# Kernel optimization log

Measured on AMD Instinct MI355X. Metric: run time of the kernel, lower is better.

## Reference

```python
import jax, jax.numpy as jnp
import numpy as np

B, S, D = 4, 1024, 1024
H, DK, DV = 16, 64, 64


def setup_inputs() -> dict:
    key = jax.random.key(0)
    ks = jax.random.split(key, 8)
    sc = 0.02
    return {
        "queries": jax.random.normal(ks[0], (B, S, D), jnp.float32),
        "keys": jax.random.normal(ks[1], (B, S, D), jnp.float32),
        "values": jax.random.normal(ks[2], (B, S, D), jnp.float32),
        "attn_bias": jax.random.normal(ks[3], (B, 1, S, S), jnp.float32),
        "Wq": jax.random.normal(ks[4], (H * DK, D), jnp.float32) * sc,
        "Wk": jax.random.normal(ks[5], (H * DK, D), jnp.float32) * sc,
        "Wv": jax.random.normal(ks[6], (H * DV, D), jnp.float32) * sc,
        "Wp": jax.random.normal(ks[7], (D, H * DV), jnp.float32) * sc,
    }


def reference(queries, keys, values, attn_bias, Wq, Wk, Wv, Wp):
    # Linear (no bias): x @ W.T, then split heads -> [B, H, S, d]
    q = (queries @ Wq.T).reshape(B, S, H, DK).transpose(0, 2, 1, 3)
    k = (keys @ Wk.T).reshape(B, S, H, DK).transpose(0, 2, 1, 3)
    v = (values @ Wv.T).reshape(B, S, H, DV).transpose(0, 2, 1, 3)
    # NOTE: original scales by d_model**-0.5, not d_key**-0.5
    scores = jnp.einsum("bhqd,bhkd->bhqk", q, k) * (D ** -0.5)
    scores = scores + attn_bias  # bias broadcasts over heads
    weights = jax.nn.softmax(scores, axis=-1)
    out = jnp.einsum("bhqk,bhkd->bhqd", weights, v)  # [B,H,S,DV]
    out = out.transpose(0, 2, 1, 3).reshape(B, S, H * DV)
    return out @ Wp.T
```

## Files before the change

### kernel.cpp

```cpp
#include <hip/hip_runtime.h>
#include <hip/hip_bf16.h>

typedef unsigned short u16;
typedef unsigned int u32;
typedef __attribute__((ext_vector_type(8))) short bf16x8;
typedef __attribute__((ext_vector_type(8))) u16 u16x8;
typedef __attribute__((ext_vector_type(4))) u16 u16x4;
typedef __attribute__((ext_vector_type(4))) u32 u32x4;
typedef __attribute__((ext_vector_type(4))) float f32x4;
typedef __attribute__((ext_vector_type(4))) _Float16 f16x4;
typedef __attribute__((ext_vector_type(16))) float f32x16;

typedef const __attribute__((address_space(1))) void* gas1_t;
typedef __attribute__((address_space(3))) void* las3_t;

#define MFMA16(a,b,c) __builtin_amdgcn_mfma_f32_16x16x32_bf16((a),(b),(c),0,0,0)
#define MFMA32(a,b,c) __builtin_amdgcn_mfma_f32_32x32x16_bf16((a),(b),(c),0,0,0)

static constexpr int BB = 4, SS = 1024, DD = 1024, HH = 16;

static __device__ __forceinline__ u16 f2b(float x) {
  union { __hip_bfloat16 h; u16 u; } cv;
  cv.h = __float2bfloat16(x);
  return cv.u;
}
static __device__ __forceinline__ u32 pk2(float a, float b) {
  return (u32)f2b(a) | ((u32)f2b(b) << 16);
}

__global__ __launch_bounds__(256) void cvt_all(
    const float* __restrict__ q, const float* __restrict__ k, const float* __restrict__ v,
    const float* __restrict__ wq_, const float* __restrict__ wk_, const float* __restrict__ wv_,
    const float* __restrict__ wp_,
    u16* __restrict__ qb, u16* __restrict__ kb, u16* __restrict__ vb,
    u16* __restrict__ wqb, u16* __restrict__ wkb, u16* __restrict__ wvb, u16* __restrict__ wpb) {
  int bid = blockIdx.x;
  const float* s; u16* d; int off;
  if      (bid < 4096)  { s = q;   d = qb;  off = bid; }
  else if (bid < 8192)  { s = k;   d = kb;  off = bid - 4096; }
  else if (bid < 12288) { s = v;   d = vb;  off = bid - 8192; }
  else if (bid < 13312) { s = wq_; d = wqb; off = bid - 12288; }
  else if (bid < 14336) { s = wk_; d = wkb; off = bid - 13312; }
  else if (bid < 15360) { s = wv_; d = wvb; off = bid - 14336; }
  else                  { s = wp_; d = wpb; off = bid - 15360; }
  int i = (off * 256 + threadIdx.x) * 4;
  float4 val = *(const float4*)(s + i);
  u16x4 r = { f2b(val.x), f2b(val.y), f2b(val.z), f2b(val.w) };
  *(u16x4*)(d + i) = r;
}

__global__ __launch_bounds__(256) void cvt_bias(const float* __restrict__ src,
                                                _Float16* __restrict__ dst) {
  int i = (blockIdx.x * 256 + threadIdx.x) * 4;
  float4 v = *(const float4*)(src + i);
  f16x4 r = { (_Float16)v.x, (_Float16)v.y, (_Float16)v.z, (_Float16)v.w };
  *(f16x4*)(dst + i) = r;
}

template<typename OT, bool VTRANS>
__global__ __launch_bounds__(256) void gemm_bt(
    const u16* __restrict__ Abase, const u16* __restrict__ Wbase, OT* __restrict__ Cbase,
    u16* __restrict__ Tout, int N, int K, size_t sA, size_t sW, size_t sC) {
  const u16* A = Abase + (size_t)blockIdx.z * sA;
  const u16* W = Wbase + (size_t)blockIdx.z * sW;
  OT* C = Cbase + (size_t)blockIdx.z * sC;

  __shared__ __align__(16) u16 As[128 * 64];
  __shared__ __align__(16) u16 Bs[128 * 64];

  const int tid = threadIdx.x;
  const int lane = tid & 63;
  const int wid = tid >> 6;
  const int g = lane >> 4;
  const int li = lane & 15;

  const int hw = blockIdx.x + (blockIdx.y << 3);
  const int L = ((hw & 7) << 5) + (hw >> 3);
  const int brow = (L >> 3) * 128;
  const int bcol = (L & 7) * 128;

  const int wr = (wid >> 1) * 64;
  const int wc = (wid & 1) * 64;

  const int srow = wid * 8 + (lane >> 3);
  const int schunk = (lane & 7) ^ (lane >> 3);
  const u16* ga0 = A + (size_t)(brow + srow) * K + schunk * 8;
  const u16* gw0 = W + (size_t)(bcol + srow) * K + schunk * 8;

  f32x4 acc[4][4] = {};

  for (int k0 = 0; k0 < K; k0 += 64) {
#pragma unroll
    for (int i = 0; i < 4; ++i) {
      __builtin_amdgcn_global_load_lds((gas1_t)(const void*)(ga0 + (size_t)(i * 32) * K + k0),
                                       (las3_t)(void*)(As + (i * 32 + wid * 8) * 64), 16, 0, 0);
      __builtin_amdgcn_global_load_lds((gas1_t)(const void*)(gw0 + (size_t)(i * 32) * K + k0),
                                       (las3_t)(void*)(Bs + (i * 32 + wid * 8) * 64), 16, 0, 0);
    }
    __syncthreads();

#pragma unroll
    for (int kk = 0; kk < 2; ++kk) {
      bf16x8 a[4], b[4];
#pragma unroll
      for (int m = 0; m < 4; ++m) {
        int row = wr + m * 16 + li;
        a[m] = *(const bf16x8*)&As[row * 64 + (((kk * 4 + g) ^ (li & 7)) << 3)];
      }
#pragma unroll
      for (int n = 0; n < 4; ++n) {
        int row = wc + n * 16 + li;
        b[n] = *(const bf16x8*)&Bs[row * 64 + (((kk * 4 + g) ^ (li & 7)) << 3)];
      }
#pragma unroll
      for (int m = 0; m < 4; ++m)
#pragma unroll
        for (int n = 0; n < 4; ++n)
          acc[m][n] = MFMA16(a[m], b[n], acc[m][n]);
    }
    __syncthreads();
  }

  if (VTRANS && blockIdx.z == 2) {
#pragma unroll
    for (int m = 0; m < 4; ++m) {
#pragma unroll
      for (int n = 0; n < 4; ++n) {
        int c = bcol + wc + n * 16 + li;
        int h_ = c >> 6, dv = c & 63;
        int r0 = brow + wr + m * 16 + g * 4;
        int b_ = r0 >> 10, s0 = r0 & 1023;
        u16x4 val = { f2b(acc[m][n][0]), f2b(acc[m][n][1]),
                      f2b(acc[m][n][2]), f2b(acc[m][n][3]) };
        *(u16x4*)&Tout[(size_t)((b_ * HH + h_) * 64 + dv) * SS + s0] = val;
      }
    }
  } else {
#pragma unroll
    for (int m = 0; m < 4; ++m)
#pragma unroll
      for (int n = 0; n < 4; ++n)
#pragma unroll
        for (int j = 0; j < 4; ++j) {
          int r = brow + wr + m * 16 + g * 4 + j;
          int c = bcol + wc + n * 16 + li;
          if constexpr (sizeof(OT) == 2) C[(size_t)r * N + c] = (OT)f2b(acc[m][n][j]);
          else                           C[(size_t)r * N + c] = acc[m][n][j];
        }
  }
}

__global__ __launch_bounds__(256) void attn_kernel(
    const u16* __restrict__ Q, const u16* __restrict__ K, const u16* __restrict__ Vt,
    const _Float16* __restrict__ bias16, u16* __restrict__ O) {
  __shared__ __align__(16) u16 kbuf[2][64 * 64];
  __shared__ __align__(16) u16 vbuf[2][64 * 64];
  __shared__ __align__(16) u16 bbuf[2][8192];

  const int tid = threadIdx.x;
  const int lane = tid & 63;
  const int wq = tid >> 6;
  const int hi = lane >> 5;
  const int ln = lane & 31;
  const u32 swz = (u32)(ln & 7) << 4;

  const int flat = blockIdx.x + (blockIdx.y << 3) + (blockIdx.z << 7);
  const int L = ((flat & 7) << 6) | (flat >> 3);
  const int qt = L & 7, h = (L >> 3) & 15, b = L >> 7;
  const int q0 = qt * 128;
  const int qrow = q0 + wq * 32 + ln;

  bf16x8 qf[4];
  {
    const u16* qp = Q + (size_t)(b * SS + qrow) * DD + h * 64 + hi * 8;
#pragma unroll
    for (int d = 0; d < 4; ++d) qf[d] = *(const bf16x8*)(qp + d * 16);
  }

  const int sr = tid >> 2;
  const int scb = (tid & 3) * 32;
  const u16* kg = K + (size_t)(b * SS + sr) * DD + h * 64 + scb / 2;
  const u16* vg = Vt + (size_t)((b * HH + h) * 64 + sr) * SS + scb / 2;
  const u32 wa0 = (u32)sr * 128 + (((u32)scb) ^ ((u32)(sr & 7) << 4));
  const u32 wa1 = (u32)sr * 128 + (((u32)scb + 16) ^ ((u32)(sr & 7) << 4));

  const int r_l = lane >> 3;
  const int gl = (lane & 7) ^ r_l;
  const _Float16* bsrc = bias16 + (size_t)(b * SS + q0 + wq * 8 + r_l) * SS + gl * 8;

  const int qq = wq * 32 + ln;
  int baddr[2][4];
#pragma unroll
  for (int kb = 0; kb < 2; ++kb)
#pragma unroll
    for (int rq = 0; rq < 4; ++rq)
      baddr[kb][rq] = qq * 128 + (((kb * 4 + rq) ^ (ln & 7)) << 4) + hi * 8;

  {
    char* bd = (char*)bbuf[0] + wq * 1024;
#pragma unroll
    for (int i = 0; i < 4; ++i)
      __builtin_amdgcn_global_load_lds((gas1_t)(const void*)(bsrc + (size_t)i * 32 * SS),
                                       (las3_t)(void*)(bd + i * 4096), 16, 0, 0);
  }
  u16x8 kr0, kr1, vr0, vr1;
  kr0 = *(const u16x8*)(kg + 0);
  kr1 = *(const u16x8*)(kg + 8);
  vr0 = *(const u16x8*)(vg + 0);
  vr1 = *(const u16x8*)(vg + 8);
  *(u16x8*)((char*)kbuf[0] + wa0) = kr0;
  *(u16x8*)((char*)kbuf[0] + wa1) = kr1;
  *(u16x8*)((char*)vbuf[0] + wa0) = vr0;
  *(u16x8*)((char*)vbuf[0] + wa1) = vr1;
  __syncthreads();

  f32x16 o0 = {}, o1 = {};
  float m = -1e30f, lsum = 0.f;
  int cur = 0;

  for (int kt = 0; kt < 16; ++kt) {
    if (kt < 15) {
      char* bd = (char*)bbuf[cur ^ 1] + wq * 1024;
      const _Float16* bs = bsrc + (kt + 1) * 64;
#pragma unroll
      for (int i = 0; i < 4; ++i)
        __builtin_amdgcn_global_load_lds((gas1_t)(const void*)(bs + (size_t)i * 32 * SS),
                                         (las3_t)(void*)(bd + i * 4096), 16, 0, 0);
      const size_t k1 = (size_t)(kt + 1) * 64;
      kr0 = *(const u16x8*)(kg + k1 * DD + 0);
      kr1 = *(const u16x8*)(kg + k1 * DD + 8);
      vr0 = *(const u16x8*)(vg + k1 + 0);
      vr1 = *(const u16x8*)(vg + k1 + 8);
    }

    const char* kb_base = (const char*)kbuf[cur];
    f32x16 s[2];
#pragma unroll
    for (int kb = 0; kb < 2; ++kb) {
      f32x16 acc = {};
#pragma unroll
      for (int d = 0; d < 4; ++d) {
        bf16x8 kf = *(const bf16x8*)(kb_base + (kb * 32 + ln) * 128 + (((u32)(d * 32 + hi * 16)) ^ swz));
        acc = MFMA32(kf, qf[d], acc);
      }
      s[kb] = acc;
    }

    const char* bbr = (const char*)bbuf[cur];
#pragma unroll
    for (int kb = 0; kb < 2; ++kb)
#pragma unroll
      for (int rq = 0; rq < 4; ++rq) {
        f16x4 bv = *(const f16x4*)(bbr + baddr[kb][rq]);
#pragma unroll
        for (int c = 0; c < 4; ++c)
          s[kb][rq * 4 + c] = fmaf(s[kb][rq * 4 + c], 0.03125f, (float)bv[c]);
      }

    float mt = -1e30f;
#pragma unroll
    for (int r = 0; r < 16; ++r) { mt = fmaxf(mt, s[0][r]); mt = fmaxf(mt, s[1][r]); }
    mt = fmaxf(mt, __shfl_xor(mt, 32));

    bool resc = false;
    float fsc = 1.f;
    if (kt == 0) {
      m = mt;
    } else if (__any(mt > m + 8.f)) {
      float mn = fmaxf(m, mt);
      fsc = __expf(m - mn);
      m = mn;
      resc = true;
    }

    float rs = 0.f;
    u32 wv[2][8];
#pragma unroll
    for (int kb = 0; kb < 2; ++kb)
#pragma unroll
      for (int t = 0; t < 8; ++t) {
        float p0 = __expf(s[kb][2 * t] - m);
        float p1 = __expf(s[kb][2 * t + 1] - m);
        rs += p0 + p1;
        wv[kb][t] = pk2(p0, p1);
      }
    rs += __shfl_xor(rs, 32);
    lsum = lsum * fsc + rs;

    if (resc) {
#pragma unroll
      for (int j = 0; j < 16; ++j) {
        float fv = __shfl(fsc, (j & 3) + 8 * (j >> 2) + 4 * hi);
        o0[j] *= fv; o1[j] *= fv;
      }
    }

    const char* vb_base = (const char*)vbuf[cur];
#pragma unroll
    for (int ks = 0; ks < 4; ++ks) {
      const int kb = ks >> 1, i0 = (ks & 1) * 4;
      u32 sA = hi ? wv[kb][i0 + 0] : wv[kb][i0 + 2];
      u32 sB = hi ? wv[kb][i0 + 1] : wv[kb][i0 + 3];
      u32 rA = (u32)__shfl_xor((int)sA, 32);
      u32 rB = (u32)__shfl_xor((int)sB, 32);
      u32 e0 = hi ? rA : wv[kb][i0 + 0];
      u32 e1 = hi ? rB : wv[kb][i0 + 1];
      u32 e2 = hi ? wv[kb][i0 + 2] : rA;
      u32 e3 = hi ? wv[kb][i0 + 3] : rB;
      union { u32x4 u; bf16x8 v; } pc;
      pc.u = (u32x4){e0, e1, e2, e3};
      bf16x8 pa = pc.v;
#pragma unroll
      for (int nv = 0; nv < 2; ++nv) {
        bf16x8 vf = *(const bf16x8*)(vb_base + (nv * 32 + ln) * 128 + (((u32)(ks * 32 + hi * 16)) ^ swz));
        if (nv == 0) o0 = MFMA32(pa, vf, o0);
        else         o1 = MFMA32(pa, vf, o1);
      }
    }

    if (kt < 15) {
      char* kd = (char*)kbuf[cur ^ 1];
      char* vd = (char*)vbuf[cur ^ 1];
      *(u16x8*)(kd + wa0) = kr0;
      *(u16x8*)(kd + wa1) = kr1;
      *(u16x8*)(vd + wa0) = vr0;
      *(u16x8*)(vd + wa1) = vr1;
      __syncthreads();
      cur ^= 1;
    }
  }

  float inv = 1.0f / lsum;
#pragma unroll
  for (int j = 0; j < 16; ++j) {
    float iv = __shfl(inv, (j & 3) + 8 * (j >> 2) + 4 * hi);
    int q = q0 + wq * 32 + (j & 3) + 8 * (j >> 2) + 4 * hi;
    u16* op = O + (size_t)(b * SS + q) * DD + h * 64 + ln;
    op[0]  = f2b(o0[j] * iv);
    op[32] = f2b(o1[j] * iv);
  }
}

extern "C" void kernel_launch(void* const* d_in, const int* in_sizes, int n_in,
                              void* d_out, int out_size, void* d_ws, size_t ws_size,
                              hipStream_t stream) {
  const float* queries = (const float*)d_in[0];
  const float* keys    = (const float*)d_in[1];
  const float* values  = (const float*)d_in[2];
  const float* bias    = (const float*)d_in[3];
  const float* Wq      = (const float*)d_in[4];
  const float* Wk      = (const float*)d_in[5];
  const float* Wv      = (const float*)d_in[6];
  const float* Wp      = (const float*)d_in[7];
  float* out = (float*)d_out;

  char* ws = (char*)d_ws;
  const size_t MB = 1024 * 1024;
  u16* qb  = (u16*)(ws + 0 * MB);
  u16* kb  = (u16*)(ws + 8 * MB);
  u16* vb  = (u16*)(ws + 16 * MB);
  u16* wqb = (u16*)(ws + 24 * MB);
  u16* wkb = (u16*)(ws + 26 * MB);
  u16* wvb = (u16*)(ws + 28 * MB);
  u16* wpb = (u16*)(ws + 30 * MB);
  u16* Qb  = (u16*)(ws + 32 * MB);
  u16* Kb  = (u16*)(ws + 40 * MB);
  u16* Vtb = (u16*)(ws + 56 * MB);
  _Float16* bias16 = (_Float16*)(ws + 8 * MB);
  u16* Ob  = (u16*)(ws + 0 * MB);

  const int nAct = BB * SS * DD;
  const int nW = DD * DD;

  cvt_all<<<dim3(16384), dim3(256), 0, stream>>>(
      queries, keys, values, Wq, Wk, Wv, Wp,
      qb, kb, vb, wqb, wkb, wvb, wpb);

  gemm_bt<u16, true><<<dim3(8, 32, 3), dim3(256), 0, stream>>>(
      qb, wqb, Qb, Vtb, DD, DD, (size_t)nAct, (size_t)nW, (size_t)nAct);

  cvt_bias<<<dim3(4096), dim3(256), 0, stream>>>(bias, bias16);

  attn_kernel<<<dim3(8, 16, 4), dim3(256), 0, stream>>>(Qb, Kb, Vtb, bias16, Ob);

  gemm_bt<float, false><<<dim3(8, 32, 1), dim3(256), 0, stream>>>(
      Ob, wpb, out, nullptr, DD, DD, 0, 0, 0);
}
```

Before: 118.1 us.

## Load K/V tiles via direct global-to-LDS and pre-permute bias layout

K and V tiles are now fetched with global_load_lds straight into shared memory using a swizzled lane mapping, instead of staging through registers and writing to LDS at the end of each iteration. The bias conversion kernel now writes fp16 bias in a permuted, swizzled order so the attention kernel can read 8 halves per LDS load instead of 4. This removes register pressure and VALU/LDS-store work from the inner loop and halves bias LDS reads. It depends on the new bias layout matching the MFMA accumulator ordering exactly.

```diff
diff --git a/kernel.cpp b/kernel.cpp
--- a/kernel.cpp
+++ b/kernel.cpp
@@ -9,6 +9,7 @@
 typedef __attribute__((ext_vector_type(4))) u32 u32x4;
 typedef __attribute__((ext_vector_type(4))) float f32x4;
 typedef __attribute__((ext_vector_type(4))) _Float16 f16x4;
+typedef __attribute__((ext_vector_type(8))) _Float16 f16x8;
 typedef __attribute__((ext_vector_type(16))) float f32x16;
 
 typedef const __attribute__((address_space(1))) void* gas1_t;
@@ -52,9 +53,16 @@
 __global__ __launch_bounds__(256) void cvt_bias(const float* __restrict__ src,
                                                 _Float16* __restrict__ dst) {
   int i = (blockIdx.x * 256 + threadIdx.x) * 4;
+  int row = i >> 10;
+  int k = i & 1023;
+  int kt = k >> 6, j = k & 63;
+  int hi = (j >> 2) & 1, kb = j >> 5, rq = (j >> 3) & 3;
+  int idx = hi * 32 + kb * 16 + rq * 4;
+  int byte_in_slice = ((((idx >> 3) ^ (row & 7)) << 4) | ((idx & 7) << 1));
   float4 v = *(const float4*)(src + i);
   f16x4 r = { (_Float16)v.x, (_Float16)v.y, (_Float16)v.z, (_Float16)v.w };
-  *(f16x4*)(dst + i) = r;
+  char* p = (char*)dst + ((size_t)row * 1024 + kt * 64) * 2 + byte_in_slice;
+  *(f16x4*)p = r;
 }
 
 template<typename OT, bool VTRANS>
@@ -177,41 +185,35 @@
     for (int d = 0; d < 4; ++d) qf[d] = *(const bf16x8*)(qp + d * 16);
   }
 
-  const int sr = tid >> 2;
-  const int scb = (tid & 3) * 32;
-  const u16* kg = K + (size_t)(b * SS + sr) * DD + h * 64 + scb / 2;
-  const u16* vg = Vt + (size_t)((b * HH + h) * 64 + sr) * SS + scb / 2;
-  const u32 wa0 = (u32)sr * 128 + (((u32)scb) ^ ((u32)(sr & 7) << 4));
-  const u32 wa1 = (u32)sr * 128 + (((u32)scb + 16) ^ ((u32)(sr & 7) << 4));
-
-  const int r_l = lane >> 3;
-  const int gl = (lane & 7) ^ r_l;
-  const _Float16* bsrc = bias16 + (size_t)(b * SS + q0 + wq * 8 + r_l) * SS + gl * 8;
+  const int srow = (lane >> 3);
+  const int spc = ((lane & 7) ^ srow) * 8;
+  const u16* kgl = K + (size_t)(b * SS + wq * 16 + srow) * DD + h * 64 + spc;
+  const u16* vgl = Vt + (size_t)((b * HH + h) * 64 + wq * 16 + srow) * SS + spc;
+
+  const _Float16* bgl = bias16 + (size_t)(b * SS + q0 + wq * 32 + srow) * SS + (lane & 7) * 8;
 
   const int qq = wq * 32 + ln;
-  int baddr[2][4];
-#pragma unroll
-  for (int kb = 0; kb < 2; ++kb)
-#pragma unroll
-    for (int rq = 0; rq < 4; ++rq)
-      baddr[kb][rq] = qq * 128 + (((kb * 4 + rq) ^ (ln & 7)) << 4) + hi * 8;
+  int baddr[4];
+#pragma unroll
+  for (int g = 0; g < 4; ++g)
+    baddr[g] = qq * 128 + (((hi * 4 + g) ^ (ln & 7)) << 4);
 
   {
-    char* bd = (char*)bbuf[0] + wq * 1024;
+    char* bd = (char*)bbuf[0] + wq * 4096;
 #pragma unroll
     for (int i = 0; i < 4; ++i)
-      __builtin_amdgcn_global_load_lds((gas1_t)(const void*)(bsrc + (size_t)i * 32 * SS),
-                                       (las3_t)(void*)(bd + i * 4096), 16, 0, 0);
-  }
-  u16x8 kr0, kr1, vr0, vr1;
-  kr0 = *(const u16x8*)(kg + 0);
-  kr1 = *(const u16x8*)(kg + 8);
-  vr0 = *(const u16x8*)(vg + 0);
-  vr1 = *(const u16x8*)(vg + 8);
-  *(u16x8*)((char*)kbuf[0] + wa0) = kr0;
-  *(u16x8*)((char*)kbuf[0] + wa1) = kr1;
-  *(u16x8*)((char*)vbuf[0] + wa0) = vr0;
-  *(u16x8*)((char*)vbuf[0] + wa1) = vr1;
+      __builtin_amdgcn_global_load_lds((gas1_t)(const void*)(bgl + (size_t)(i * 8) * SS),
+                                       (las3_t)(void*)(bd + i * 1024), 16, 0, 0);
+    char* kd = (char*)kbuf[0] + wq * 2048;
+    char* vd = (char*)vbuf[0] + wq * 2048;
+#pragma unroll
+    for (int j = 0; j < 2; ++j) {
+      __builtin_amdgcn_global_load_lds((gas1_t)(const void*)(kgl + (size_t)(j * 8) * DD),
+                                       (las3_t)(void*)(kd + j * 1024), 16, 0, 0);
+      __builtin_amdgcn_global_load_lds((gas1_t)(const void*)(vgl + (size_t)(j * 8) * SS),
+                                       (las3_t)(void*)(vd + j * 1024), 16, 0, 0);
+    }
+  }
   __syncthreads();
 
   f32x16 o0 = {}, o1 = {};
@@ -220,17 +222,22 @@
 
   for (int kt = 0; kt < 16; ++kt) {
     if (kt < 15) {
-      char* bd = (char*)bbuf[cur ^ 1] + wq * 1024;
-      const _Float16* bs = bsrc + (kt + 1) * 64;
+      char* bd = (char*)bbuf[cur ^ 1] + wq * 4096;
+      const _Float16* bs = bgl + (kt + 1) * 64;
 #pragma unroll
       for (int i = 0; i < 4; ++i)
-        __builtin_amdgcn_global_load_lds((gas1_t)(const void*)(bs + (size_t)i * 32 * SS),
-                                         (las3_t)(void*)(bd + i * 4096), 16, 0, 0);
+        __builtin_amdgcn_global_load_lds((gas1_t)(const void*)(bs + (size_t)(i * 8) * SS),
+                                         (las3_t)(void*)(bd + i * 1024), 16, 0, 0);
+      char* kd = (char*)kbuf[cur ^ 1] + wq * 2048;
+      char* vd = (char*)vbuf[cur ^ 1] + wq * 2048;
       const size_t k1 = (size_t)(kt + 1) * 64;
-      kr0 = *(const u16x8*)(kg + k1 * DD + 0);
-      kr1 = *(const u16x8*)(kg + k1 * DD + 8);
-      vr0 = *(const u16x8*)(vg + k1 + 0);
-      vr1 = *(const u16x8*)(vg + k1 + 8);
+#pragma unroll
+      for (int j = 0; j < 2; ++j) {
+        __builtin_amdgcn_global_load_lds((gas1_t)(const void*)(kgl + (k1 + j * 8) * DD),
+                                         (las3_t)(void*)(kd + j * 1024), 16, 0, 0);
+        __builtin_amdgcn_global_load_lds((gas1_t)(const void*)(vgl + (size_t)(j * 8) * SS + k1),
+                                         (las3_t)(void*)(vd + j * 1024), 16, 0, 0);
+      }
     }
 
     const char* kb_base = (const char*)kbuf[cur];
@@ -246,16 +253,18 @@
       s[kb] = acc;
     }
 
-    const char* bbr = (const char*)bbuf[cur];
-#pragma unroll
-    for (int kb = 0; kb < 2; ++kb)
-#pragma unroll
-      for (int rq = 0; rq < 4; ++rq) {
-        f16x4 bv = *(const f16x4*)(bbr + baddr[kb][rq]);
-#pragma unroll
-        for (int c = 0; c < 4; ++c)
-          s[kb][rq * 4 + c] = fmaf(s[kb][rq * 4 + c], 0.03125f, (float)bv[c]);
-      }
+    {
+      const char* bbr = (const char*)bbuf[cur];
+#pragma unroll
+      for (int g = 0; g < 4; ++g) {
+        f16x8 bv = *(const f16x8*)(bbr + baddr[g]);
+        const int kb = g >> 1, rq0 = (g & 1) * 2;
+#pragma unroll
+        for (int e = 0; e < 8; ++e)
+          s[kb][(rq0 + (e >> 2)) * 4 + (e & 3)] =
+              fmaf(s[kb][(rq0 + (e >> 2)) * 4 + (e & 3)], 0.03125f, (float)bv[e]);
+      }
+    }
 
     float mt = -1e30f;
 #pragma unroll
@@ -319,12 +328,6 @@
     }
 
     if (kt < 15) {
-      char* kd = (char*)kbuf[cur ^ 1];
-      char* vd = (char*)vbuf[cur ^ 1];
-      *(u16x8*)(kd + wa0) = kr0;
-      *(u16x8*)(kd + wa1) = kr1;
-      *(u16x8*)(vd + wa0) = vr0;
-      *(u16x8*)(vd + wa1) = vr1;
       __syncthreads();
       cur ^= 1;
     }
```

Measured after the change: 119.5 us. About the same (+1.3%).
